# Performance work log

Hardware: AMD Instinct MI355X
Metric: run time of the kernel (lower is better)

Reference implementation:

```python
import jax, jax.numpy as jnp
import numpy as np

B, T, C, H = 4, 2048, 1024, 16
D = C // H  # head dim = 64


def setup_inputs() -> dict:
    key = jax.random.key(0)
    ks = jax.random.split(key, 5)
    s = 1.0 / np.sqrt(C)
    return {
        "x": jax.random.normal(ks[0], (B, T, C), jnp.float32),
        "Wq": jax.random.normal(ks[1], (C, C), jnp.float32) * s,
        "bq": jnp.zeros((C,), jnp.float32),
        "Wk": jax.random.normal(ks[2], (C, C), jnp.float32) * s,
        "bk": jnp.zeros((C,), jnp.float32),
        "Wv": jax.random.normal(ks[3], (C, C), jnp.float32) * s,
        "bv": jnp.zeros((C,), jnp.float32),
        "Wp": jax.random.normal(ks[4], (C, C), jnp.float32) * s,
        "bp": jnp.zeros((C,), jnp.float32),
    }


def reference(x, Wq, bq, Wk, bk, Wv, bv, Wp, bp):
    # linear projections -> [B, H, T, D]
    def heads(t):
        return t.reshape(B, T, H, D).transpose(0, 2, 1, 3)
    q = heads(x @ Wq.T + bq)
    k = heads(x @ Wk.T + bk)
    v = heads(x @ Wv.T + bv)
    scale = 1.0 / np.sqrt(D)
    att = jnp.einsum("bhtd,bhsd->bhts", q, k) * scale  # [B,H,T,T]
    causal = jnp.tril(jnp.ones((T, T), bool))
    att = jnp.where(causal[None, None], att, -jnp.inf)
    att = jax.nn.softmax(att, axis=-1)
    y = jnp.einsum("bhts,bhsd->bhtd", att, v)  # [B,H,T,D]
    y = y.transpose(0, 2, 1, 3).reshape(B, T, C)
    return y @ Wp.T + bp
```

## Files before the change

kernel.cpp:

```cpp
#include <hip/hip_runtime.h>

typedef float f32x4 __attribute__((ext_vector_type(4)));
typedef __bf16 bf16x8 __attribute__((ext_vector_type(8)));
typedef unsigned short u16x8 __attribute__((ext_vector_type(8)));

#define SCQ 0.1803368801111183f

__device__ inline unsigned short f2bf(float f) {
  unsigned int u = __builtin_bit_cast(unsigned int, f);
  u += 0x7FFFu + ((u >> 16) & 1u);
  return (unsigned short)(u >> 16);
}
__device__ inline unsigned short f2bf_fast(float f) {
  unsigned int u = __builtin_bit_cast(unsigned int, f);
  return (unsigned short)((u + 0x8000u) >> 16);
}

__device__ inline float fexp2(float x) {
#if __has_builtin(__builtin_amdgcn_exp2f)
  return __builtin_amdgcn_exp2f(x);
#else
  return exp2f(x);
#endif
}

template <int N>
__device__ inline float rowror(float v) {
  return __builtin_bit_cast(float, __builtin_amdgcn_update_dpp(
      0, __builtin_bit_cast(int, v), 0x120 | N, 0xF, 0xF, true));
}
__device__ inline float rowsum16(float v) {
  v += rowror<8>(v); v += rowror<4>(v);
  v += rowror<2>(v); v += rowror<1>(v);
  return v;
}

__device__ inline void gload_lds16(const unsigned short* g, unsigned short* l) {
  __builtin_amdgcn_global_load_lds(
      (const __attribute__((address_space(1))) unsigned int*)g,
      (__attribute__((address_space(3))) unsigned int*)l, 16, 0, 0);
}

__global__ void cvt_x(const float* __restrict__ in, unsigned short* __restrict__ out) {
  int i = (blockIdx.x * 256 + threadIdx.x) * 4;
  float4 f = *(const float4*)(in + i);
  ushort4 o;
  o.x = f2bf(f.x); o.y = f2bf(f.y); o.z = f2bf(f.z); o.w = f2bf(f.w);
  *(ushort4*)(out + i) = o;
}

__global__ void cvt_w(const float* __restrict__ a, const float* __restrict__ b,
                      const float* __restrict__ c, const float* __restrict__ d,
                      unsigned short* __restrict__ oa, unsigned short* __restrict__ ob,
                      unsigned short* __restrict__ oc, unsigned short* __restrict__ od) {
  const float* src[4] = {a, b, c, d};
  unsigned short* dst[4] = {oa, ob, oc, od};
  int m = blockIdx.y;
  int i = (blockIdx.x * 256 + threadIdx.x) * 4;
  float4 f = *(const float4*)(src[m] + i);
  ushort4 o;
  o.x = f2bf(f.x); o.y = f2bf(f.y); o.z = f2bf(f.z); o.w = f2bf(f.w);
  *(ushort4*)(dst[m] + i) = o;
}

template <int MODE>
__global__ __launch_bounds__(256) void gemm128(const unsigned short* __restrict__ A,
                                               const unsigned short* __restrict__ Bt,
                                               const float* __restrict__ b0,
                                               const float* __restrict__ b1,
                                               const float* __restrict__ b2,
                                               void* __restrict__ out,
                                               int M, int N, int K) {
  __shared__ __align__(16) unsigned short As[128 * 64];
  __shared__ __align__(16) unsigned short Bs[128 * 64];
  const int tid = threadIdx.x;
  const int lane = tid & 63, w = tid >> 6;
  const int quad = lane >> 4, l15 = lane & 15;
  const int wm = w & 1, wn = w >> 1;
  const int m0 = blockIdx.x * 128, n0 = blockIdx.y * 128;

  f32x4 acc[4][4] = {};

  for (int kb = 0; kb < K; kb += 64) {
#pragma unroll
    for (int j = 0; j < 4; j++) {
      int ch = j * 256 + w * 64 + lane;
      int row = ch >> 3, pc = ch & 7;
      int c = pc ^ (row & 7);
      gload_lds16(A + (size_t)(m0 + row) * K + kb + c * 8, As + (size_t)(j * 256 + w * 64) * 8);
      gload_lds16(Bt + (size_t)(n0 + row) * K + kb + c * 8, Bs + (size_t)(j * 256 + w * 64) * 8);
    }
    __syncthreads();
#pragma unroll
    for (int ks = 0; ks < 64; ks += 32) {
      bf16x8 af[4], bf[4];
#pragma unroll
      for (int mt = 0; mt < 4; mt++) {
        int row = wm * 64 + mt * 16 + l15;
        int pc = ((ks >> 3) + quad) ^ (row & 7);
        af[mt] = *(const bf16x8*)(As + row * 64 + pc * 8);
      }
#pragma unroll
      for (int nt = 0; nt < 4; nt++) {
        int row = wn * 64 + nt * 16 + l15;
        int pc = ((ks >> 3) + quad) ^ (row & 7);
        bf[nt] = *(const bf16x8*)(Bs + row * 64 + pc * 8);
      }
#pragma unroll
      for (int mt = 0; mt < 4; mt++)
#pragma unroll
        for (int nt = 0; nt < 4; nt++)
          acc[mt][nt] = __builtin_amdgcn_mfma_f32_16x16x32_bf16(af[mt], bf[nt], acc[mt][nt], 0, 0, 0);
    }
    __syncthreads();
  }

#pragma unroll
  for (int mt = 0; mt < 4; mt++)
#pragma unroll
    for (int nt = 0; nt < 4; nt++) {
      int col = n0 + wn * 64 + nt * 16 + l15;
      float bv, sc;
      int which = 0, cl = col;
      if (MODE == 0) {
        which = col >> 10; cl = col & 1023;
        const float* bp = (which == 0) ? b0 : ((which == 1) ? b1 : b2);
        bv = bp[cl];
        sc = (which == 0) ? SCQ : 1.f;
      } else {
        bv = b0[col]; sc = 1.f;
      }
#pragma unroll
      for (int r = 0; r < 4; r++) {
        int row = m0 + wm * 64 + mt * 16 + quad * 4 + r;
        float v = (acc[mt][nt][r] + bv) * sc;
        if (MODE == 0) {
          int h = cl >> 6, d = cl & 63;
          int b = row >> 11, t = row & 2047;
          ((unsigned short*)out)[(size_t)which * 8388608 +
                                 ((size_t)((b * 16 + h) * 2048 + t)) * 64 + d] = f2bf(v);
        } else {
          ((float*)out)[(size_t)row * N + col] = v;
        }
      }
    }
}

__global__ __launch_bounds__(256) void transpose_v(const unsigned short* __restrict__ V,
                                                   unsigned short* __restrict__ Vt) {
  constexpr int P = 66;
  __shared__ unsigned short L[64 * P];
  const int tid = threadIdx.x;
  const int bh = blockIdx.y;
  const int t0 = blockIdx.x * 64;
  const unsigned short* Vp = V + (size_t)bh * 2048 * 64;
  unsigned short* Op = Vt + (size_t)bh * 64 * 2048;
#pragma unroll
  for (int j = 0; j < 2; j++) {
    int r = (tid >> 3) + j * 32;
    int c = (tid & 7) * 8;
    u16x8 v = *(const u16x8*)(Vp + (size_t)(t0 + r) * 64 + c);
#pragma unroll
    for (int i = 0; i < 4; i++) {
      unsigned int pk = (unsigned int)v[2 * i] | ((unsigned int)v[2 * i + 1] << 16);
      *(unsigned int*)&L[r * P + c + 2 * i] = pk;
    }
  }
  __syncthreads();
#pragma unroll
  for (int j = 0; j < 2; j++) {
    int ch = j * 256 + tid;
    int d = ch >> 3, tc = (ch & 7) * 8;
    u16x8 o;
#pragma unroll
    for (int k = 0; k < 8; k++) o[k] = L[(tc + k) * P + d];
    *(u16x8*)(Op + (size_t)d * 2048 + t0 + tc) = o;
  }
}

__global__ __launch_bounds__(256, 4) void attn_kernel(const unsigned short* __restrict__ Q,
                                                      const unsigned short* __restrict__ Km,
                                                      const unsigned short* __restrict__ Vt,
                                                      unsigned short* __restrict__ Y) {
  constexpr int T = 2048, D = 64;
  constexpr int PP = 72;
  __shared__ __align__(16) unsigned short Ks[64 * 64];
  __shared__ __align__(16) unsigned short Vs[64 * 64];
  __shared__ __align__(16) unsigned short P_lds[4][16 * PP];
  const int tid = threadIdx.x;
  const int lane = tid & 63, w = tid >> 6;
  const int quad = lane >> 4, l15 = lane & 15;
  const int bh = blockIdx.y;
  const int b = bh >> 4, h = bh & 15;
  const int p = blockIdx.x;
  const unsigned short* Qp = Q + (size_t)bh * T * D;
  const unsigned short* Kp = Km + (size_t)bh * T * D;
  const unsigned short* Vp = Vt + (size_t)bh * D * T;
  unsigned short* pl = P_lds[w];

  const int bch0 = (w * 2) * 64, bch1 = (w * 2 + 1) * 64;
  const int ch0 = bch0 + lane, ch1 = bch1 + lane;
  const int row0 = ch0 >> 3, c0 = (ch0 & 7) ^ (row0 & 7);
  const int row1 = ch1 >> 3, c1 = (ch1 & 7) ^ (row1 & 7);

  for (int phase = 0; phase < 2; ++phase) {
    const int jt = phase ? (127 - (p * 4 + w)) : (p * 4 + w);
    const int qt = jt * 16;
    const int send = qt + 15;
    const int nit = phase ? (32 - p) : (p + 1);

    bf16x8 aq[2];
    aq[0] = *(const bf16x8*)(Qp + (size_t)(qt + l15) * D + quad * 8);
    aq[1] = *(const bf16x8*)(Qp + (size_t)(qt + l15) * D + 32 + quad * 8);

    f32x4 o[4] = {};
    float lrow[4] = {0.f, 0.f, 0.f, 0.f};

    for (int it = 0; it < nit; ++it) {
      const int s0 = it * 64;
      gload_lds16(Kp + (size_t)(s0 + row0) * 64 + c0 * 8, Ks + (size_t)bch0 * 8);
      gload_lds16(Kp + (size_t)(s0 + row1) * 64 + c1 * 8, Ks + (size_t)bch1 * 8);
      gload_lds16(Vp + (size_t)row0 * T + s0 + c0 * 8, Vs + (size_t)bch0 * 8);
      gload_lds16(Vp + (size_t)row1 * T + s0 + c1 * 8, Vs + (size_t)bch1 * 8);
      __syncthreads();

      const bool full = (s0 + 63) <= qt;
      const int nsc = full ? 4 : (((send - s0) >> 4) + 1);
      const int nsc2 = (nsc + 1) & ~1;

#pragma unroll
      for (int sc = 0; sc < 4; sc++) {
        if (sc < nsc) {
          f32x4 s = {};
#pragma unroll
          for (int kh = 0; kh < 2; kh++) {
            int kr = sc * 16 + l15;
            int pc = (kh * 4 + quad) ^ (kr & 7);
            u16x8 bku = *(const u16x8*)(Ks + kr * 64 + pc * 8);
            s = __builtin_amdgcn_mfma_f32_16x16x32_bf16(aq[kh], __builtin_bit_cast(bf16x8, bku), s, 0, 0, 0);
          }
          if (full) {
#pragma unroll
            for (int r = 0; r < 4; r++) {
              float e = fexp2(s[r]);
              lrow[r] += e;
              pl[(quad * 4 + r) * PP + sc * 16 + l15] = f2bf_fast(e);
            }
          } else {
            int sg = s0 + sc * 16 + l15;
#pragma unroll
            for (int r = 0; r < 4; r++) {
              float e = fexp2(s[r]);
              e = (sg > qt + quad * 4 + r) ? 0.f : e;
              lrow[r] += e;
              pl[(quad * 4 + r) * PP + sc * 16 + l15] = f2bf_fast(e);
            }
          }
        } else if (sc < nsc2) {
#pragma unroll
          for (int r = 0; r < 4; r++)
            pl[(quad * 4 + r) * PP + sc * 16 + l15] = 0;
        }
      }
      __asm__ __volatile__("" ::: "memory");
#pragma unroll
      for (int h2 = 0; h2 < 2; h2++) {
        if (h2 * 2 < nsc2) {
          u16x8 apu = *(const u16x8*)(pl + l15 * PP + h2 * 32 + quad * 8);
          bf16x8 ap = __builtin_bit_cast(bf16x8, apu);
#pragma unroll
          for (int dc = 0; dc < 4; dc++) {
            int vr = dc * 16 + l15;
            int pc = (h2 * 4 + quad) ^ (vr & 7);
            u16x8 vu = *(const u16x8*)(Vs + vr * 64 + pc * 8);
            o[dc] = __builtin_amdgcn_mfma_f32_16x16x32_bf16(ap, __builtin_bit_cast(bf16x8, vu), o[dc], 0, 0, 0);
          }
        }
      }
      __syncthreads();
    }

#pragma unroll
    for (int r = 0; r < 4; r++) {
      float inv = 1.f / rowsum16(lrow[r]);
      int qg = qt + quad * 4 + r;
#pragma unroll
      for (int dc = 0; dc < 4; dc++)
        Y[((size_t)(b * T + qg)) * 1024 + h * 64 + dc * 16 + l15] = f2bf(o[dc][r] * inv);
    }
  }
}

extern "C" void kernel_launch(void* const* d_in, const int* in_sizes, int n_in,
                              void* d_out, int out_size, void* d_ws, size_t ws_size,
                              hipStream_t stream) {
  const float* x  = (const float*)d_in[0];
  const float* Wq = (const float*)d_in[1];
  const float* bq = (const float*)d_in[2];
  const float* Wk = (const float*)d_in[3];
  const float* bk = (const float*)d_in[4];
  const float* Wv = (const float*)d_in[5];
  const float* bv = (const float*)d_in[6];
  const float* Wp = (const float*)d_in[7];
  const float* bp = (const float*)d_in[8];

  char* ws = (char*)d_ws;
  unsigned short* xb  = (unsigned short*)(ws + 0);
  unsigned short* wqb = (unsigned short*)(ws + 16777216);
  unsigned short* wkb = (unsigned short*)(ws + 18874368);
  unsigned short* wvb = (unsigned short*)(ws + 20971520);
  unsigned short* wpb = (unsigned short*)(ws + 23068672);
  unsigned short* Qb  = (unsigned short*)(ws + 25165824);
  unsigned short* Kb  = (unsigned short*)(ws + 41943040);
  unsigned short* Vb  = (unsigned short*)(ws + 58720256);
  unsigned short* Vtb = xb;
  unsigned short* Yb  = Vb;

  cvt_x<<<8192, 256, 0, stream>>>(x, xb);
  cvt_w<<<dim3(1024, 4), 256, 0, stream>>>(Wq, Wk, Wv, Wp, wqb, wkb, wvb, wpb);

  gemm128<0><<<dim3(64, 24), 256, 0, stream>>>(xb, wqb, bq, bk, bv, Qb, 8192, 3072, 1024);

  transpose_v<<<dim3(32, 64), 256, 0, stream>>>(Vb, Vtb);
  attn_kernel<<<dim3(16, 64), 256, 0, stream>>>(Qb, Kb, Vtb, Yb);

  gemm128<1><<<dim3(64, 8), 256, 0, stream>>>(Yb, wpb, bp, bp, bp, d_out, 8192, 1024, 1024);
}
```

Before: 279.6 us.

## Use 32x32 MFMA in GEMMs and double-buffer K/V with two query tiles per wave

The projection GEMMs move from 16x16x32 to 32x32x16 bf16 MFMA tiles, which cuts the number of LDS fragment reads per MFMA. The attention kernel now double-buffers K/V tiles in LDS, prefetching the next tile while computing the current one. Each wave handles two 16-row query tiles, so every loaded K/V tile is reused twice, and the grid is halved. The cost is more LDS and registers (launch bounds lowered to 2 blocks) and fewer blocks, which could lower occupancy or leave parallelism unused.

```diff
diff --git a/kernel.cpp b/kernel.cpp
--- a/kernel.cpp
+++ b/kernel.cpp
@@ -1,6 +1,7 @@
 #include <hip/hip_runtime.h>
 
 typedef float f32x4 __attribute__((ext_vector_type(4)));
+typedef float f32x16 __attribute__((ext_vector_type(16)));
 typedef __bf16 bf16x8 __attribute__((ext_vector_type(8)));
 typedef unsigned short u16x8 __attribute__((ext_vector_type(8)));
 
@@ -75,11 +76,11 @@
   __shared__ __align__(16) unsigned short Bs[128 * 64];
   const int tid = threadIdx.x;
   const int lane = tid & 63, w = tid >> 6;
-  const int quad = lane >> 4, l15 = lane & 15;
+  const int l31 = lane & 31, half = lane >> 5;
   const int wm = w & 1, wn = w >> 1;
   const int m0 = blockIdx.x * 128, n0 = blockIdx.y * 128;
 
-  f32x4 acc[4][4] = {};
+  f32x16 acc[2][2] = {};
 
   for (int kb = 0; kb < K; kb += 64) {
 #pragma unroll
@@ -92,34 +93,34 @@
     }
     __syncthreads();
 #pragma unroll
-    for (int ks = 0; ks < 64; ks += 32) {
-      bf16x8 af[4], bf[4];
-#pragma unroll
-      for (int mt = 0; mt < 4; mt++) {
-        int row = wm * 64 + mt * 16 + l15;
-        int pc = ((ks >> 3) + quad) ^ (row & 7);
-        af[mt] = *(const bf16x8*)(As + row * 64 + pc * 8);
-      }
-#pragma unroll
-      for (int nt = 0; nt < 4; nt++) {
-        int row = wn * 64 + nt * 16 + l15;
-        int pc = ((ks >> 3) + quad) ^ (row & 7);
-        bf[nt] = *(const bf16x8*)(Bs + row * 64 + pc * 8);
-      }
-#pragma unroll
-      for (int mt = 0; mt < 4; mt++)
-#pragma unroll
-        for (int nt = 0; nt < 4; nt++)
-          acc[mt][nt] = __builtin_amdgcn_mfma_f32_16x16x32_bf16(af[mt], bf[nt], acc[mt][nt], 0, 0, 0);
+    for (int ks = 0; ks < 64; ks += 16) {
+      bf16x8 af[2], bfr[2];
+#pragma unroll
+      for (int at = 0; at < 2; at++) {
+        int row = wm * 64 + at * 32 + l31;
+        int pc = ((ks >> 3) + half) ^ (row & 7);
+        af[at] = *(const bf16x8*)(As + row * 64 + pc * 8);
+      }
+#pragma unroll
+      for (int nt = 0; nt < 2; nt++) {
+        int row = wn * 64 + nt * 32 + l31;
+        int pc = ((ks >> 3) + half) ^ (row & 7);
+        bfr[nt] = *(const bf16x8*)(Bs + row * 64 + pc * 8);
+      }
+#pragma unroll
+      for (int at = 0; at < 2; at++)
+#pragma unroll
+        for (int nt = 0; nt < 2; nt++)
+          acc[at][nt] = __builtin_amdgcn_mfma_f32_32x32x16_bf16(af[at], bfr[nt], acc[at][nt], 0, 0, 0);
     }
     __syncthreads();
   }
 
 #pragma unroll
-  for (int mt = 0; mt < 4; mt++)
-#pragma unroll
-    for (int nt = 0; nt < 4; nt++) {
-      int col = n0 + wn * 64 + nt * 16 + l15;
+  for (int at = 0; at < 2; at++)
+#pragma unroll
+    for (int nt = 0; nt < 2; nt++) {
+      int col = n0 + wn * 64 + nt * 32 + l31;
       float bv, sc;
       int which = 0, cl = col;
       if (MODE == 0) {
@@ -131,9 +132,9 @@
         bv = b0[col]; sc = 1.f;
       }
 #pragma unroll
-      for (int r = 0; r < 4; r++) {
-        int row = m0 + wm * 64 + mt * 16 + quad * 4 + r;
-        float v = (acc[mt][nt][r] + bv) * sc;
+      for (int reg = 0; reg < 16; reg++) {
+        int row = m0 + wm * 64 + at * 32 + (reg & 3) + 8 * (reg >> 2) + 4 * half;
+        float v = (acc[at][nt][reg] + bv) * sc;
         if (MODE == 0) {
           int h = cl >> 6, d = cl & 63;
           int b = row >> 11, t = row & 2047;
@@ -178,15 +179,74 @@
   }
 }
 
-__global__ __launch_bounds__(256, 4) void attn_kernel(const unsigned short* __restrict__ Q,
+#define PPITCH 72
+__device__ __attribute__((always_inline)) inline
+void attn_tile(int qt, int s0, const bf16x8* aq, const unsigned short* Ks,
+               const unsigned short* Vs, unsigned short* pl,
+               f32x4* o, float* lrow, int quad, int l15) {
+  const bool full = (s0 + 63) <= qt;
+  const int nsc = full ? 4 : (((qt + 15 - s0) >> 4) + 1);
+  const int nsc2 = (nsc + 1) & ~1;
+
+#pragma unroll
+  for (int sc = 0; sc < 4; sc++) {
+    if (sc < nsc) {
+      f32x4 s = {};
+#pragma unroll
+      for (int kh = 0; kh < 2; kh++) {
+        int kr = sc * 16 + l15;
+        int pc = (kh * 4 + quad) ^ (kr & 7);
+        u16x8 bku = *(const u16x8*)(Ks + kr * 64 + pc * 8);
+        s = __builtin_amdgcn_mfma_f32_16x16x32_bf16(aq[kh], __builtin_bit_cast(bf16x8, bku), s, 0, 0, 0);
+      }
+      if (full) {
+#pragma unroll
+        for (int r = 0; r < 4; r++) {
+          float e = fexp2(s[r]);
+          lrow[r] += e;
+          pl[(quad * 4 + r) * PPITCH + sc * 16 + l15] = f2bf_fast(e);
+        }
+      } else {
+        int sg = s0 + sc * 16 + l15;
+#pragma unroll
+        for (int r = 0; r < 4; r++) {
+          float e = fexp2(s[r]);
+          e = (sg > qt + quad * 4 + r) ? 0.f : e;
+          lrow[r] += e;
+          pl[(quad * 4 + r) * PPITCH + sc * 16 + l15] = f2bf_fast(e);
+        }
+      }
+    } else if (sc < nsc2) {
+#pragma unroll
+      for (int r = 0; r < 4; r++)
+        pl[(quad * 4 + r) * PPITCH + sc * 16 + l15] = 0;
+    }
+  }
+  __asm__ __volatile__("" ::: "memory");
+#pragma unroll
+  for (int h2 = 0; h2 < 2; h2++) {
+    if (h2 * 2 < nsc2) {
+      u16x8 apu = *(const u16x8*)(pl + l15 * PPITCH + h2 * 32 + quad * 8);
+      bf16x8 ap = __builtin_bit_cast(bf16x8, apu);
+#pragma unroll
+      for (int dc = 0; dc < 4; dc++) {
+        int vr = dc * 16 + l15;
+        int pc = (h2 * 4 + quad) ^ (vr & 7);
+        u16x8 vu = *(const u16x8*)(Vs + vr * 64 + pc * 8);
+        o[dc] = __builtin_amdgcn_mfma_f32_16x16x32_bf16(ap, __builtin_bit_cast(bf16x8, vu), o[dc], 0, 0, 0);
+      }
+    }
+  }
+}
+
+__global__ __launch_bounds__(256, 2) void attn_kernel(const unsigned short* __restrict__ Q,
                                                       const unsigned short* __restrict__ Km,
                                                       const unsigned short* __restrict__ Vt,
                                                       unsigned short* __restrict__ Y) {
   constexpr int T = 2048, D = 64;
-  constexpr int PP = 72;
-  __shared__ __align__(16) unsigned short Ks[64 * 64];
-  __shared__ __align__(16) unsigned short Vs[64 * 64];
-  __shared__ __align__(16) unsigned short P_lds[4][16 * PP];
+  __shared__ __align__(16) unsigned short Ks[2][64 * 64];
+  __shared__ __align__(16) unsigned short Vs[2][64 * 64];
+  __shared__ __align__(16) unsigned short P_lds[4][16 * PPITCH];
   const int tid = threadIdx.x;
   const int lane = tid & 63, w = tid >> 6;
   const int quad = lane >> 4, l15 = lane & 15;
@@ -204,89 +264,53 @@
   const int row1 = ch1 >> 3, c1 = (ch1 & 7) ^ (row1 & 7);
 
   for (int phase = 0; phase < 2; ++phase) {
-    const int jt = phase ? (127 - (p * 4 + w)) : (p * 4 + w);
-    const int qt = jt * 16;
-    const int send = qt + 15;
-    const int nit = phase ? (32 - p) : (p + 1);
-
-    bf16x8 aq[2];
-    aq[0] = *(const bf16x8*)(Qp + (size_t)(qt + l15) * D + quad * 8);
-    aq[1] = *(const bf16x8*)(Qp + (size_t)(qt + l15) * D + 32 + quad * 8);
-
-    f32x4 o[4] = {};
-    float lrow[4] = {0.f, 0.f, 0.f, 0.f};
+    int jlo, jhi;
+    if (!phase) { jlo = 8 * p + w; jhi = jlo + 4; }
+    else        { jhi = 127 - 8 * p - w; jlo = jhi - 4; }
+    const int qlo = jlo * 16, qhi = jhi * 16;
+    const int nit = phase ? (32 - 2 * p) : (2 * p + 2);
+
+    bf16x8 aqlo[2], aqhi[2];
+    aqlo[0] = *(const bf16x8*)(Qp + (size_t)(qlo + l15) * D + quad * 8);
+    aqlo[1] = *(const bf16x8*)(Qp + (size_t)(qlo + l15) * D + 32 + quad * 8);
+    aqhi[0] = *(const bf16x8*)(Qp + (size_t)(qhi + l15) * D + quad * 8);
+    aqhi[1] = *(const bf16x8*)(Qp + (size_t)(qhi + l15) * D + 32 + quad * 8);
+
+    f32x4 olo[4] = {}, ohi[4] = {};
+    float llo[4] = {0.f, 0.f, 0.f, 0.f}, lhi[4] = {0.f, 0.f, 0.f, 0.f};
+
+    gload_lds16(Kp + (size_t)row0 * 64 + c0 * 8, Ks[0] + (size_t)bch0 * 8);
+    gload_lds16(Kp + (size_t)row1 * 64 + c1 * 8, Ks[0] + (size_t)bch1 * 8);
+    gload_lds16(Vp + (size_t)row0 * T + c0 * 8, Vs[0] + (size_t)bch0 * 8);
+    gload_lds16(Vp + (size_t)row1 * T + c1 * 8, Vs[0] + (size_t)bch1 * 8);
+    __syncthreads();
 
     for (int it = 0; it < nit; ++it) {
       const int s0 = it * 64;
-      gload_lds16(Kp + (size_t)(s0 + row0) * 64 + c0 * 8, Ks + (size_t)bch0 * 8);
-      gload_lds16(Kp + (size_t)(s0 + row1) * 64 + c1 * 8, Ks + (size_t)bch1 * 8);
-      gload_lds16(Vp + (size_t)row0 * T + s0 + c0 * 8, Vs + (size_t)bch0 * 8);
-      gload_lds16(Vp + (size_t)row1 * T + s0 + c1 * 8, Vs + (size_t)bch1 * 8);
+      const int cur = it & 1, nxt = cur ^ 1;
+      if (it + 1 < nit) {
+        const int sn = s0 + 64;
+        gload_lds16(Kp + (size_t)(sn + row0) * 64 + c0 * 8, Ks[nxt] + (size_t)bch0 * 8);
+        gload_lds16(Kp + (size_t)(sn + row1) * 64 + c1 * 8, Ks[nxt] + (size_t)bch1 * 8);
+        gload_lds16(Vp + (size_t)row0 * T + sn + c0 * 8, Vs[nxt] + (size_t)bch0 * 8);
+        gload_lds16(Vp + (size_t)row1 * T + sn + c1 * 8, Vs[nxt] + (size_t)bch1 * 8);
+      }
+      if (s0 <= qlo + 15)
+        attn_tile(qlo, s0, aqlo, Ks[cur], Vs[cur], pl, olo, llo, quad, l15);
+      attn_tile(qhi, s0, aqhi, Ks[cur], Vs[cur], pl, ohi, lhi, quad, l15);
       __syncthreads();
-
-      const bool full = (s0 + 63) <= qt;
-      const int nsc = full ? 4 : (((send - s0) >> 4) + 1);
-      const int nsc2 = (nsc + 1) & ~1;
-
-#pragma unroll
-      for (int sc = 0; sc < 4; sc++) {
-        if (sc < nsc) {
-          f32x4 s = {};
-#pragma unroll
-          for (int kh = 0; kh < 2; kh++) {
-            int kr = sc * 16 + l15;
-            int pc = (kh * 4 + quad) ^ (kr & 7);
-            u16x8 bku = *(const u16x8*)(Ks + kr * 64 + pc * 8);
-            s = __builtin_amdgcn_mfma_f32_16x16x32_bf16(aq[kh], __builtin_bit_cast(bf16x8, bku), s, 0, 0, 0);
-          }
-          if (full) {
-#pragma unroll
-            for (int r = 0; r < 4; r++) {
-              float e = fexp2(s[r]);
-              lrow[r] += e;
-              pl[(quad * 4 + r) * PP + sc * 16 + l15] = f2bf_fast(e);
-            }
-          } else {
-            int sg = s0 + sc * 16 + l15;
-#pragma unroll
-            for (int r = 0; r < 4; r++) {
-              float e = fexp2(s[r]);
-              e = (sg > qt + quad * 4 + r) ? 0.f : e;
-              lrow[r] += e;
-              pl[(quad * 4 + r) * PP + sc * 16 + l15] = f2bf_fast(e);
-            }
-          }
-        } else if (sc < nsc2) {
-#pragma unroll
-          for (int r = 0; r < 4; r++)
-            pl[(quad * 4 + r) * PP + sc * 16 + l15] = 0;
-        }
-      }
-      __asm__ __volatile__("" ::: "memory");
-#pragma unroll
-      for (int h2 = 0; h2 < 2; h2++) {
-        if (h2 * 2 < nsc2) {
-          u16x8 apu = *(const u16x8*)(pl + l15 * PP + h2 * 32 + quad * 8);
-          bf16x8 ap = __builtin_bit_cast(bf16x8, apu);
-#pragma unroll
-          for (int dc = 0; dc < 4; dc++) {
-            int vr = dc * 16 + l15;
-            int pc = (h2 * 4 + quad) ^ (vr & 7);
-            u16x8 vu = *(const u16x8*)(Vs + vr * 64 + pc * 8);
-            o[dc] = __builtin_amdgcn_mfma_f32_16x16x32_bf16(ap, __builtin_bit_cast(bf16x8, vu), o[dc], 0, 0, 0);
-          }
-        }
-      }
-      __syncthreads();
     }
 
 #pragma unroll
     for (int r = 0; r < 4; r++) {
-      float inv = 1.f / rowsum16(lrow[r]);
-      int qg = qt + quad * 4 + r;
-#pragma unroll
-      for (int dc = 0; dc < 4; dc++)
-        Y[((size_t)(b * T + qg)) * 1024 + h * 64 + dc * 16 + l15] = f2bf(o[dc][r] * inv);
+      float ilo = 1.f / rowsum16(llo[r]);
+      float ihi = 1.f / rowsum16(lhi[r]);
+      int glo = qlo + quad * 4 + r, ghi = qhi + quad * 4 + r;
+#pragma unroll
+      for (int dc = 0; dc < 4; dc++) {
+        Y[((size_t)(b * T + glo)) * 1024 + h * 64 + dc * 16 + l15] = f2bf(olo[dc][r] * ilo);
+        Y[((size_t)(b * T + ghi)) * 1024 + h * 64 + dc * 16 + l15] = f2bf(ohi[dc][r] * ihi);
+      }
     }
   }
 }
@@ -322,7 +346,7 @@
   gemm128<0><<<dim3(64, 24), 256, 0, stream>>>(xb, wqb, bq, bk, bv, Qb, 8192, 3072, 1024);
 
   transpose_v<<<dim3(32, 64), 256, 0, stream>>>(Vb, Vtb);
-  attn_kernel<<<dim3(16, 64), 256, 0, stream>>>(Qb, Kb, Vtb, Yb);
+  attn_kernel<<<dim3(8, 64), 256, 0, stream>>>(Qb, Kb, Vtb, Yb);
 
   gemm128<1><<<dim3(64, 8), 256, 0, stream>>>(Yb, wpb, bp, bp, bp, d_out, 8192, 1024, 1024);
 }
```

Measured after the change: 281.3 us. Within noise of the previous version (+0.6%).
